# Kernel optimization log

Measured on AMD Instinct MI355X. Metric: run time of the kernel, lower is better.

The kernel has to match this reference:

```python
import jax, jax.numpy as jnp
import numpy as np

N = 100000      # nodes
E = 1600000     # edges (before self-loops)
F_IN = 128
H1, C1 = 8, 8   # layer 1: 8 heads x 8 channels
H2, C2 = 1, 64  # layer 2: 1 head x 64 channels
NEG_SLOPE = 0.2


def setup_inputs() -> dict:
    key = jax.random.key(0)
    ks = jax.random.split(key, 10)
    x = jax.random.normal(ks[0], (N, F_IN), jnp.float32)
    edge_index = jax.random.randint(ks[1], (2, E), 0, N, dtype=jnp.int32)
    s1 = 1.0 / np.sqrt(F_IN)
    s2 = 1.0 / np.sqrt(H1 * C1)
    return {
        "x": x,
        "edge_index": edge_index,
        "W1": jax.random.normal(ks[2], (F_IN, H1 * C1), jnp.float32) * s1,
        "a_src1": jax.random.normal(ks[3], (H1, C1), jnp.float32) * s1,
        "a_dst1": jax.random.normal(ks[4], (H1, C1), jnp.float32) * s1,
        "b1": jnp.zeros((H1 * C1,), jnp.float32),
        "W2": jax.random.normal(ks[5], (H1 * C1, H2 * C2), jnp.float32) * s2,
        "a_src2": jax.random.normal(ks[6], (H2, C2), jnp.float32) * s2,
        "a_dst2": jax.random.normal(ks[7], (H2, C2), jnp.float32) * s2,
        "b2": jnp.zeros((C2,), jnp.float32),
    }


def gat_conv(x, W, a_src, a_dst, b, src, dst, heads, out_ch, concat):
    """PyG-style GATConv (eval mode, self-loops already in src/dst)."""
    n = x.shape[0]
    h = (x @ W).reshape(n, heads, out_ch)            # [N, H, C]
    alpha_s = jnp.sum(h * a_src, axis=-1)            # [N, H]
    alpha_d = jnp.sum(h * a_dst, axis=-1)            # [N, H]
    e = alpha_s[src] + alpha_d[dst]                  # [E, H]
    e = jnp.where(e > 0, e, NEG_SLOPE * e)           # leaky relu
    # segment softmax grouped by destination node
    m = jax.ops.segment_max(e, dst, num_segments=n)  # [N, H]
    m = jnp.where(jnp.isfinite(m), m, 0.0)
    p = jnp.exp(e - m[dst])                          # [E, H]
    denom = jax.ops.segment_sum(p, dst, num_segments=n)
    alpha = p / (denom[dst] + 1e-16)                 # [E, H]
    # weighted scatter-add aggregation
    out = jax.ops.segment_sum(h[src] * alpha[:, :, None], dst, num_segments=n)
    out = out.reshape(n, heads * out_ch) if concat else out.mean(axis=1)
    return out + b


def reference(x, edge_index, W1, a_src1, a_dst1, b1, W2, a_src2, a_dst2, b2):
    n = x.shape[0]
    loops = jnp.arange(n, dtype=edge_index.dtype)    # PyG adds self-loops
    src = jnp.concatenate([edge_index[0], loops])
    dst = jnp.concatenate([edge_index[1], loops])
    h = gat_conv(x, W1, a_src1, a_dst1, b1, src, dst, H1, C1, True)
    h = jax.nn.elu(h)
    h = gat_conv(h, W2, a_src2, a_dst2, b2, src, dst, H2, C2, False)
    return jax.nn.log_softmax(h, axis=1)
```

## Files before the change

### kernel.cpp

```cpp
#include <hip/hip_runtime.h>
#include <math.h>

#define NEG_SLOPE 0.2f
#define CHUNK 4096
#define NPART 128
#define SLICECAP 80
#define CAP 48

typedef __attribute__((ext_vector_type(8))) short bf16x8;
typedef __attribute__((ext_vector_type(4))) float f32x4;

__device__ __forceinline__ unsigned short f2bf(float f) {
    unsigned int u = __float_as_uint(f);
    unsigned int r = (u + 0x7FFFu + ((u >> 16) & 1u)) >> 16;
    return (unsigned short)r;
}
__device__ __forceinline__ float bfl(unsigned int u) { return __uint_as_float(u << 16); }
__device__ __forceinline__ float bfh(unsigned int u) { return __uint_as_float(u & 0xffff0000u); }

__global__ void bucket_slice(const int* __restrict__ ei, int E, int nchunks, int PR,
                             int2* __restrict__ qds, int* __restrict__ scnt) {
    __shared__ int lcnt[8][NPART];
    __shared__ int lbase[8][NPART];
    int tid = threadIdx.x, wave = tid >> 6;
    int chunk = blockIdx.x;
    int base = chunk * CHUNK;
    for (int i = tid; i < 8 * NPART; i += 512) ((int*)lcnt)[i] = 0;
    __syncthreads();
    int d[8], s[8], b[8], pos[8];
    #pragma unroll
    for (int k = 0; k < 8; ++k) {
        int t = base + k * 512 + tid;
        bool v = t < E;
        d[k] = v ? ei[E + t] : 0;
        s[k] = v ? ei[t] : 0;
        b[k] = v ? (d[k] / PR) : -1;
    }
    #pragma unroll
    for (int k = 0; k < 8; ++k)
        pos[k] = (b[k] >= 0) ? atomicAdd(&lcnt[wave][b[k]], 1) : 0;
    __syncthreads();
    if (tid < NPART) {
        int run = 0;
        #pragma unroll
        for (int w = 0; w < 8; ++w) { lbase[w][tid] = run; run += lcnt[w][tid]; }
        scnt[tid * nchunks + chunk] = run;
    }
    __syncthreads();
    #pragma unroll
    for (int k = 0; k < 8; ++k) {
        if (b[k] >= 0) {
            int p = lbase[wave][b[k]] + pos[k];
            if (p < SLICECAP)
                qds[(size_t)(b[k] * nchunks + chunk) * SLICECAP + p] = make_int2(d[k], s[k]);
        }
    }
}

__global__ void scatter_lds(const int2* __restrict__ qds, const int* __restrict__ scnt,
                            int nchunks, int PR, int N,
                            int* __restrict__ cnt, int* __restrict__ col) {
    extern __shared__ int lc[];
    int b = blockIdx.x;
    int lo = b * PR;
    int tid = threadIdx.x, lane = tid & 63, wave = tid >> 6;
    int nwaves = blockDim.x >> 6;
    for (int i = tid; i < PR; i += blockDim.x) lc[i] = 0;
    __syncthreads();
    for (int sl = wave; sl < nchunks; sl += nwaves) {
        int n = min(scnt[b * nchunks + sl], SLICECAP);
        const int2* q = qds + (size_t)(b * nchunks + sl) * SLICECAP;
        for (int i = lane; i < n; i += 64) {
            int2 e = q[i];
            int p = atomicAdd(&lc[e.x - lo], 1);
            if (p < CAP - 1)
                col[e.x * CAP + p] = e.y;
        }
    }
    __syncthreads();
    for (int i = tid; i < PR; i += blockDim.x) {
        int d = lo + i;
        if (d < N) {
            int p = min(lc[i], CAP - 1);
            col[d * CAP + p] = d;
            cnt[d] = p + 1;
        }
    }
}

template<int K, int H, typename AT>
__global__ __launch_bounds__(256) void gemm_mfma(const AT* __restrict__ A,
                                                 const float* __restrict__ W,
                                                 unsigned short* __restrict__ Hb,
                                                 const float* __restrict__ a_src,
                                                 const float* __restrict__ a_dst,
                                                 float* __restrict__ AS,
                                                 float* __restrict__ AD, int N) {
    constexpr int LD = K + 8;
    __shared__ __align__(16) unsigned short Wt[64 * LD];
    __shared__ __align__(16) unsigned short Xl[64 * LD];
    const int tid = threadIdx.x;
    const int lane = tid & 63, wave = tid >> 6;
    const int l16 = lane & 15, q = lane >> 4;
    const int lcol = (lane & 3) * 16;
    for (int i = tid; i < K * 64; i += 256) {
        int k = i >> 6, c = i & 63;
        Wt[c * LD + k] = f2bf(W[i]);
    }
    float4 asv0 = *(const float4*)&a_src[lcol];
    float4 asv1 = *(const float4*)&a_src[lcol + 4];
    float4 asv2 = *(const float4*)&a_src[lcol + 8];
    float4 asv3 = *(const float4*)&a_src[lcol + 12];
    float4 adv0 = *(const float4*)&a_dst[lcol];
    float4 adv1 = *(const float4*)&a_dst[lcol + 4];
    float4 adv2 = *(const float4*)&a_dst[lcol + 8];
    float4 adv3 = *(const float4*)&a_dst[lcol + 12];
    __syncthreads();
    for (int rb = blockIdx.x; rb * 64 < N; rb += gridDim.x) {
        int r0 = rb * 64;
        if (sizeof(AT) == 4) {
            const float* Af = (const float*)A;
            for (int i = tid; i < 64 * (K / 4); i += 256) {
                int row = i / (K / 4), kq = i % (K / 4);
                int rg = min(r0 + row, N - 1);
                float4 a = *(const float4*)&Af[(size_t)rg * K + kq * 4];
                unsigned int u0 = (unsigned int)f2bf(a.x) | ((unsigned int)f2bf(a.y) << 16);
                unsigned int u1 = (unsigned int)f2bf(a.z) | ((unsigned int)f2bf(a.w) << 16);
                *(uint2*)&Xl[row * LD + kq * 4] = make_uint2(u0, u1);
            }
        } else {
            const unsigned short* Ab = (const unsigned short*)A;
            for (int i = tid; i < 64 * (K / 8); i += 256) {
                int row = i / (K / 8), k8 = i % (K / 8);
                int rg = min(r0 + row, N - 1);
                uint4 a = *(const uint4*)&Ab[(size_t)rg * K + k8 * 8];
                *(uint4*)&Xl[row * LD + k8 * 8] = a;
            }
        }
        __syncthreads();
        f32x4 acc[4] = {{0.f,0.f,0.f,0.f},{0.f,0.f,0.f,0.f},{0.f,0.f,0.f,0.f},{0.f,0.f,0.f,0.f}};
        #pragma unroll
        for (int kk = 0; kk < K / 32; ++kk) {
            bf16x8 af = *(bf16x8*)&Xl[(wave * 16 + l16) * LD + kk * 32 + q * 8];
            #pragma unroll
            for (int c = 0; c < 4; ++c) {
                bf16x8 bfr = *(bf16x8*)&Wt[(c * 16 + l16) * LD + kk * 32 + q * 8];
                acc[c] = __builtin_amdgcn_mfma_f32_16x16x32_bf16(af, bfr, acc[c], 0, 0, 0);
            }
        }
        #pragma unroll
        for (int c = 0; c < 4; ++c)
            #pragma unroll
            for (int r = 0; r < 4; ++r)
                Xl[(wave * 16 + q * 4 + r) * LD + c * 16 + l16] = f2bf(acc[c][r]);
        int lrow = wave * 16 + (lane >> 2);
        int node = r0 + lrow;
        uint4 o0 = *(uint4*)&Xl[lrow * LD + lcol];
        uint4 o1 = *(uint4*)&Xl[lrow * LD + lcol + 8];
        if (node < N) {
            *(uint4*)&Hb[(size_t)node * 64 + lcol] = o0;
            *(uint4*)&Hb[(size_t)node * 64 + lcol + 8] = o1;
            float sl = bfl(o0.x)*asv0.x + bfh(o0.x)*asv0.y + bfl(o0.y)*asv0.z + bfh(o0.y)*asv0.w
                     + bfl(o0.z)*asv1.x + bfh(o0.z)*asv1.y + bfl(o0.w)*asv1.z + bfh(o0.w)*asv1.w;
            float sh = bfl(o1.x)*asv2.x + bfh(o1.x)*asv2.y + bfl(o1.y)*asv2.z + bfh(o1.y)*asv2.w
                     + bfl(o1.z)*asv3.x + bfh(o1.z)*asv3.y + bfl(o1.w)*asv3.z + bfh(o1.w)*asv3.w;
            float dl = bfl(o0.x)*adv0.x + bfh(o0.x)*adv0.y + bfl(o0.y)*adv0.z + bfh(o0.y)*adv0.w
                     + bfl(o0.z)*adv1.x + bfh(o0.z)*adv1.y + bfl(o0.w)*adv1.z + bfh(o0.w)*adv1.w;
            float dh = bfl(o1.x)*adv2.x + bfh(o1.x)*adv2.y + bfl(o1.y)*adv2.z + bfh(o1.y)*adv2.w
                     + bfl(o1.z)*adv3.x + bfh(o1.z)*adv3.y + bfl(o1.w)*adv3.z + bfh(o1.w)*adv3.w;
            if (H == 8) {
                float2 sv = {sl, sh};
                float2 dv = {dl, dh};
                *(float2*)&AS[(size_t)node * 8 + (lane & 3) * 2] = sv;
                *(float2*)&AD[(size_t)node * 8 + (lane & 3) * 2] = dv;
            } else {
                float s = sl + sh, d = dl + dh;
                s += __shfl_xor(s, 1, 64); s += __shfl_xor(s, 2, 64);
                d += __shfl_xor(d, 1, 64); d += __shfl_xor(d, 2, 64);
                if ((lane & 3) == 0) { AS[node] = s; AD[node] = d; }
            }
        }
        __syncthreads();
    }
}

template<int H, bool FINAL>
__global__ __launch_bounds__(256, 4) void aggregate(
                          const int* __restrict__ cnt, const int* __restrict__ col,
                          const float* __restrict__ AS, const float* __restrict__ AD,
                          const uint4* __restrict__ Hb, const float* __restrict__ bias,
                          void* __restrict__ OUT, int N) {
    int lane = threadIdx.x & 63;
    int wid = (blockIdx.x * blockDim.x + threadIdx.x) >> 6;
    int nw = (gridDim.x * blockDim.x) >> 6;
    int slot = lane >> 3, l8 = lane & 7;
    const int h = (H == 8) ? l8 : 0;
    float4 b4a = *(const float4*)&bias[l8 * 8];
    float4 b4b = *(const float4*)&bias[l8 * 8 + 4];
    for (int nb0 = wid * 8; nb0 < N; nb0 += nw * 8) {
        int n = nb0 + slot;
        bool nok = n < N;
        int nc = nok ? n : (N - 1);
        int beg = nc * CAP;
        int deg = cnt[nc];
        float ad = AD[(size_t)nc * H + h];
        int maxd = deg;
        #pragma unroll
        for (int off = 8; off <= 32; off <<= 1)
            maxd = max(maxd, __shfl_xor(maxd, off, 64));
        float den = 0.0f;
        float acc[8] = {0.f, 0.f, 0.f, 0.f, 0.f, 0.f, 0.f, 0.f};
        int myc = (l8 < deg) ? col[beg + l8] : -1;
        for (int j0 = 0; j0 < maxd; j0 += 8) {
            int mnext = (j0 + 8 + l8 < deg) ? col[beg + j0 + 8 + l8] : -1;
            int sarr[8];
            #pragma unroll
            for (int jj = 0; jj < 8; ++jj)
                sarr[jj] = __shfl(myc, slot * 8 + jj, 64);
            float ev[8];
            uint4 hvv[8];
            #pragma unroll
            for (int jj = 0; jj < 8; ++jj) {
                if (sarr[jj] >= 0) {
                    ev[jj]  = AS[(size_t)sarr[jj] * H + h];
                    hvv[jj] = Hb[(size_t)sarr[jj] * 8 + l8];
                }
            }
            #pragma unroll
            for (int jj = 0; jj < 8; ++jj) {
                if (sarr[jj] >= 0) {
                    float e = ev[jj] + ad;
                    e = e > 0.0f ? e : NEG_SLOPE * e;
                    float p = __expf(e);
                    den += p;
                    uint4 hv = hvv[jj];
                    acc[0] = fmaf(p, bfl(hv.x), acc[0]);
                    acc[1] = fmaf(p, bfh(hv.x), acc[1]);
                    acc[2] = fmaf(p, bfl(hv.y), acc[2]);
                    acc[3] = fmaf(p, bfh(hv.y), acc[3]);
                    acc[4] = fmaf(p, bfl(hv.z), acc[4]);
                    acc[5] = fmaf(p, bfh(hv.z), acc[5]);
                    acc[6] = fmaf(p, bfl(hv.w), acc[6]);
                    acc[7] = fmaf(p, bfh(hv.w), acc[7]);
                }
            }
            myc = mnext;
        }
        float inv = 1.0f / (den + 1e-16f);
        float v[8];
        v[0] = acc[0] * inv + b4a.x; v[1] = acc[1] * inv + b4a.y;
        v[2] = acc[2] * inv + b4a.z; v[3] = acc[3] * inv + b4a.w;
        v[4] = acc[4] * inv + b4b.x; v[5] = acc[5] * inv + b4b.y;
        v[6] = acc[6] * inv + b4b.z; v[7] = acc[7] * inv + b4b.w;
        if (!FINAL) {
            #pragma unroll
            for (int i = 0; i < 8; ++i) v[i] = v[i] > 0.0f ? v[i] : __expf(v[i]) - 1.0f;
            if (nok) {
                union { unsigned short u[8]; uint4 q; } pk;
                #pragma unroll
                for (int i = 0; i < 8; ++i) pk.u[i] = f2bf(v[i]);
                ((uint4*)OUT)[(size_t)n * 8 + l8] = pk.q;
            }
        } else {
            float m = v[0];
            #pragma unroll
            for (int i = 1; i < 8; ++i) m = fmaxf(m, v[i]);
            #pragma unroll
            for (int off = 1; off <= 4; off <<= 1) m = fmaxf(m, __shfl_xor(m, off, 64));
            float ss = 0.0f;
            #pragma unroll
            for (int i = 0; i < 8; ++i) ss += __expf(v[i] - m);
            #pragma unroll
            for (int off = 1; off <= 4; off <<= 1) ss += __shfl_xor(ss, off, 64);
            float lse = m + __logf(ss);
            if (nok) {
                float* Of = (float*)OUT;
                float4 o0 = {v[0] - lse, v[1] - lse, v[2] - lse, v[3] - lse};
                float4 o1 = {v[4] - lse, v[5] - lse, v[6] - lse, v[7] - lse};
                *(float4*)&Of[(size_t)n * 64 + l8 * 8] = o0;
                *(float4*)&Of[(size_t)n * 64 + l8 * 8 + 4] = o1;
            }
        }
    }
}

extern "C" void kernel_launch(void* const* d_in, const int* in_sizes, int n_in,
                              void* d_out, int out_size, void* d_ws, size_t ws_size,
                              hipStream_t stream) {
    const float* x    = (const float*)d_in[0];
    const int*   ei   = (const int*)d_in[1];
    const float* W1   = (const float*)d_in[2];
    const float* as1w = (const float*)d_in[3];
    const float* ad1w = (const float*)d_in[4];
    const float* b1   = (const float*)d_in[5];
    const float* W2   = (const float*)d_in[6];
    const float* as2w = (const float*)d_in[7];
    const float* ad2w = (const float*)d_in[8];
    const float* b2   = (const float*)d_in[9];
    const int N = in_sizes[0] / 128;
    const int E = in_sizes[1] / 2;
    const int nchunks = (E + CHUNK - 1) / CHUNK;
    const int PR = (N + NPART - 1) / NPART;

    float* ws = (float*)d_ws;
    size_t off = 0;
    unsigned short* AGG1b = (unsigned short*)(ws + off); off += (size_t)N * 32;
    unsigned short* h1b   = (unsigned short*)(ws + off); off += (size_t)N * 32;
    unsigned short* h2b   = (unsigned short*)(ws + off); off += (size_t)N * 32;
    int2* qds = (int2*)ws;
    float* AS1  = ws + off; off += (size_t)N * 8;
    float* AD1  = ws + off; off += (size_t)N * 8;
    float* AS2  = ws + off; off += N;
    float* AD2  = ws + off; off += N;
    int* cnt    = (int*)(ws + off);
    int* scnt   = cnt + N;
    int* col    = scnt + NPART * nchunks;

    bucket_slice<<<nchunks, 512, 0, stream>>>(ei, E, nchunks, PR, qds, scnt);
    scatter_lds<<<NPART, 1024, PR * sizeof(int), stream>>>(qds, scnt, nchunks,
                                                           PR, N, cnt, col);

    gemm_mfma<128, 8, float><<<1563, 256, 0, stream>>>(x, W1, h1b, as1w, ad1w,
                                                       AS1, AD1, N);
    aggregate<8, false><<<1563, 256, 0, stream>>>(cnt, col, AS1, AD1,
                                                  (const uint4*)h1b, b1, AGG1b, N);
    gemm_mfma<64, 1, unsigned short><<<1563, 256, 0, stream>>>(AGG1b, W2, h2b,
                                                               as2w, ad2w, AS2, AD2, N);
    aggregate<1, true><<<1563, 256, 0, stream>>>(cnt, col, AS2, AD2,
                                                 (const uint4*)h2b, b2, d_out, N);
}
```

Measured before the change: 255.6 us.

## Fuse layer-2 linear transform and attention logits into layer-1 aggregate

Layer 1's aggregation epilogue now applies ELU and then multiplies each node's 64-wide row by W2, held in shared memory. It uses wave shuffles to broadcast the row elements, then computes the layer-2 source and destination attention scalars and writes bf16 h2 directly. This removes the separate layer-2 GEMM launch and the round trip of the intermediate AGG1 buffer through global memory. In exchange the aggregate kernel gets 16KB of LDS per block, more registers and a scalar FMA loop in place of MFMA, which may lower occupancy. Because h2 is now computed in fp32 from fp32 activations rather than from bf16-rounded inputs, results can differ slightly.

New measurement: 876.9 us. 3.43x slower.

```diff
diff --git a/kernel.cpp b/kernel.cpp
--- a/kernel.cpp
+++ b/kernel.cpp
@@ -184,12 +184,17 @@
     }
 }
 
-template<int H, bool FINAL>
+template<int H, bool FINAL, bool FUSE_W2>
 __global__ __launch_bounds__(256, 4) void aggregate(
                           const int* __restrict__ cnt, const int* __restrict__ col,
                           const float* __restrict__ AS, const float* __restrict__ AD,
                           const uint4* __restrict__ Hb, const float* __restrict__ bias,
-                          void* __restrict__ OUT, int N) {
+                          void* __restrict__ OUT,
+                          const float* __restrict__ W2g,
+                          const float* __restrict__ as2,
+                          const float* __restrict__ ad2,
+                          float* __restrict__ AS2o, float* __restrict__ AD2o, int N) {
+    __shared__ float W2l[FUSE_W2 ? 4096 : 1];
     int lane = threadIdx.x & 63;
     int wid = (blockIdx.x * blockDim.x + threadIdx.x) >> 6;
     int nw = (gridDim.x * blockDim.x) >> 6;
@@ -197,6 +202,13 @@
     const int h = (H == 8) ? l8 : 0;
     float4 b4a = *(const float4*)&bias[l8 * 8];
     float4 b4b = *(const float4*)&bias[l8 * 8 + 4];
+    float4 as2a, as2b, ad2a, ad2b;
+    if constexpr (FUSE_W2) {
+        for (int i = threadIdx.x; i < 4096; i += blockDim.x) W2l[i] = W2g[i];
+        as2a = *(const float4*)&as2[l8 * 8];  as2b = *(const float4*)&as2[l8 * 8 + 4];
+        ad2a = *(const float4*)&ad2[l8 * 8];  ad2b = *(const float4*)&ad2[l8 * 8 + 4];
+        __syncthreads();
+    }
     for (int nb0 = wid * 8; nb0 < N; nb0 += nw * 8) {
         int n = nb0 + slot;
         bool nok = n < N;
@@ -252,14 +264,41 @@
         v[2] = acc[2] * inv + b4a.z; v[3] = acc[3] * inv + b4a.w;
         v[4] = acc[4] * inv + b4b.x; v[5] = acc[5] * inv + b4b.y;
         v[6] = acc[6] * inv + b4b.z; v[7] = acc[7] * inv + b4b.w;
-        if (!FINAL) {
+        if constexpr (!FINAL) {
             #pragma unroll
             for (int i = 0; i < 8; ++i) v[i] = v[i] > 0.0f ? v[i] : __expf(v[i]) - 1.0f;
-            if (nok) {
-                union { unsigned short u[8]; uint4 q; } pk;
+            if constexpr (FUSE_W2) {
+                float h2a[8] = {0.f,0.f,0.f,0.f,0.f,0.f,0.f,0.f};
                 #pragma unroll
-                for (int i = 0; i < 8; ++i) pk.u[i] = f2bf(v[i]);
-                ((uint4*)OUT)[(size_t)n * 8 + l8] = pk.q;
+                for (int c = 0; c < 64; ++c) {
+                    float hc = __shfl(v[c & 7], slot * 8 + (c >> 3), 64);
+                    float4 w0 = *(const float4*)&W2l[c * 64 + l8 * 8];
+                    float4 w1 = *(const float4*)&W2l[c * 64 + l8 * 8 + 4];
+                    h2a[0] = fmaf(hc, w0.x, h2a[0]); h2a[1] = fmaf(hc, w0.y, h2a[1]);
+                    h2a[2] = fmaf(hc, w0.z, h2a[2]); h2a[3] = fmaf(hc, w0.w, h2a[3]);
+                    h2a[4] = fmaf(hc, w1.x, h2a[4]); h2a[5] = fmaf(hc, w1.y, h2a[5]);
+                    h2a[6] = fmaf(hc, w1.z, h2a[6]); h2a[7] = fmaf(hc, w1.w, h2a[7]);
+                }
+                float s2 = h2a[0]*as2a.x + h2a[1]*as2a.y + h2a[2]*as2a.z + h2a[3]*as2a.w
+                         + h2a[4]*as2b.x + h2a[5]*as2b.y + h2a[6]*as2b.z + h2a[7]*as2b.w;
+                float d2 = h2a[0]*ad2a.x + h2a[1]*ad2a.y + h2a[2]*ad2a.z + h2a[3]*ad2a.w
+                         + h2a[4]*ad2b.x + h2a[5]*ad2b.y + h2a[6]*ad2b.z + h2a[7]*ad2b.w;
+                s2 += __shfl_xor(s2, 1, 64); s2 += __shfl_xor(s2, 2, 64); s2 += __shfl_xor(s2, 4, 64);
+                d2 += __shfl_xor(d2, 1, 64); d2 += __shfl_xor(d2, 2, 64); d2 += __shfl_xor(d2, 4, 64);
+                if (nok) {
+                    union { unsigned short u[8]; uint4 q; } pk;
+                    #pragma unroll
+                    for (int i = 0; i < 8; ++i) pk.u[i] = f2bf(h2a[i]);
+                    ((uint4*)OUT)[(size_t)n * 8 + l8] = pk.q;
+                    if (l8 == 0) { AS2o[n] = s2; AD2o[n] = d2; }
+                }
+            } else {
+                if (nok) {
+                    union { unsigned short u[8]; uint4 q; } pk;
+                    #pragma unroll
+                    for (int i = 0; i < 8; ++i) pk.u[i] = f2bf(v[i]);
+                    ((uint4*)OUT)[(size_t)n * 8 + l8] = pk.q;
+                }
             }
         } else {
             float m = v[0];
@@ -304,7 +343,6 @@
 
     float* ws = (float*)d_ws;
     size_t off = 0;
-    unsigned short* AGG1b = (unsigned short*)(ws + off); off += (size_t)N * 32;
     unsigned short* h1b   = (unsigned short*)(ws + off); off += (size_t)N * 32;
     unsigned short* h2b   = (unsigned short*)(ws + off); off += (size_t)N * 32;
     int2* qds = (int2*)ws;
@@ -322,10 +360,11 @@
 
     gemm_mfma<128, 8, float><<<1563, 256, 0, stream>>>(x, W1, h1b, as1w, ad1w,
                                                        AS1, AD1, N);
-    aggregate<8, false><<<1563, 256, 0, stream>>>(cnt, col, AS1, AD1,
-                                                  (const uint4*)h1b, b1, AGG1b, N);
-    gemm_mfma<64, 1, unsigned short><<<1563, 256, 0, stream>>>(AGG1b, W2, h2b,
-                                                               as2w, ad2w, AS2, AD2, N);
-    aggregate<1, true><<<1563, 256, 0, stream>>>(cnt, col, AS2, AD2,
-                                                 (const uint4*)h2b, b2, d_out, N);
-}
+    aggregate<8, false, true><<<1563, 256, 0, stream>>>(cnt, col, AS1, AD1,
+                                                        (const uint4*)h1b, b1, h2b,
+                                                        W2, as2w, ad2w, AS2, AD2, N);
+    aggregate<1, true, false><<<1563, 256, 0, stream>>>(cnt, col, AS2, AD2,
+                                                        (const uint4*)h2b, b2, d_out,
+                                                        nullptr, nullptr, nullptr,
+                                                        nullptr, nullptr, N);
+}
```
